# Performance work log

Measured on AMD Instinct MI355X. Metric: run time of the kernel, lower is better.

The kernel has to match this reference:

```python
import jax, jax.numpy as jnp
import numpy as np

T, B = 2048, 16384  # sequence_length, minibatch_size

def setup_inputs() -> dict:
    key = jax.random.key(0)
    ks = jax.random.split(key, 6)
    return {
        "x": jax.random.normal(ks[0], (T, B, 1), dtype=jnp.float32),
        "W1": jax.random.normal(ks[1], (4, 2), dtype=jnp.float32) * 0.5,
        "W2": jax.random.normal(ks[2], (4, 4), dtype=jnp.float32) * 0.5,
        "b2": jax.random.normal(ks[3], (4,), dtype=jnp.float32) * 0.1,
        "W3": jax.random.normal(ks[4], (4, 4), dtype=jnp.float32) * 0.5,
        "W4": jax.random.normal(ks[5], (1, 4), dtype=jnp.float32) * 0.5,
    }

def reference(x, W1, b2, W2, W3, W4):
    # x: (T, B, 1). State starts at zeros (self.state is None -> zeros), no teacher forcing.
    def step(state, x_t):
        # state: (B, 1); x_t: (B, 1)
        inp = jnp.concatenate([x_t, state], axis=-1)        # (B, 2)
        h = jnp.tanh(inp @ W1.T)                            # (B, 4)
        h = jnp.tanh(h @ W2.T + b2)                         # (B, 4)
        h = jnp.tanh(h @ W3.T)                              # (B, 4)
        d = h @ W4.T                                        # (B, 1)
        out = d + state                                     # residual state feedback
        return out, out
    state0 = jnp.zeros((x.shape[1], 1), dtype=x.dtype)
    _, outs = jax.lax.scan(step, state0, x)                 # outs: (T, B, 1)
    return outs
```

## Files before the change

kernel.cpp:

```cpp
#include <hip/hip_runtime.h>

#define TT 2048

__device__ __forceinline__ float tanh_pre(float z) {
    float t = __builtin_amdgcn_exp2f(z);
    float r = __builtin_amdgcn_rcpf(1.0f + t);
    return fmaf(-2.0f, r, 1.0f);
}

__global__ __launch_bounds__(64, 1)
void stn_seq_kernel(const float* __restrict__ x,
                    const float* __restrict__ W1,
                    const float* __restrict__ W2,
                    const float* __restrict__ b2,
                    const float* __restrict__ W3,
                    const float* __restrict__ W4,
                    float* __restrict__ out, int B)
{
    const int b = blockIdx.x * blockDim.x + threadIdx.x;
    if (b >= B) return;
    const float K = 2.8853900817779268f;

    float w1x[4], w1s[4], w2[4][4], bb[4], w3[4][4], w4[4];
    #pragma unroll
    for (int i = 0; i < 4; ++i) {
        w1x[i] = W1[i*2+0] * K;
        w1s[i] = W1[i*2+1] * K;
        bb[i]  = b2[i] * K;
        w4[i]  = W4[i];
        #pragma unroll
        for (int j = 0; j < 4; ++j) {
            w2[i][j] = W2[i*4+j] * K;
            w3[i][j] = W3[i*4+j] * K;
        }
    }

    const float* xp = x + b;
    float* op = out + b;
    float s = 0.0f;

    constexpr int U = 4;
    float xb[U];
    #pragma unroll
    for (int k = 0; k < U; ++k) xb[k] = __builtin_nontemporal_load(xp + k*B);
    xp += (size_t)U * B;

    for (int t = 0; t < TT; t += U) {
        float xc[U];
        #pragma unroll
        for (int k = 0; k < U; ++k) xc[k] = xb[k];
        if (t + U < TT) {
            #pragma unroll
            for (int k = 0; k < U; ++k) xb[k] = __builtin_nontemporal_load(xp + k*B);
        }
        xp += (size_t)U * B;

        #pragma unroll
        for (int k = 0; k < U; ++k) {
            float h1[4], h2[4], h3[4];
            #pragma unroll
            for (int i = 0; i < 4; ++i)
                h1[i] = tanh_pre(fmaf(w1s[i], s, w1x[i] * xc[k]));
            #pragma unroll
            for (int i = 0; i < 4; ++i) {
                float a = bb[i];
                #pragma unroll
                for (int j = 0; j < 4; ++j) a = fmaf(w2[i][j], h1[j], a);
                h2[i] = tanh_pre(a);
            }
            #pragma unroll
            for (int i = 0; i < 4; ++i) {
                float a = w3[i][0] * h2[0];
                #pragma unroll
                for (int j = 1; j < 4; ++j) a = fmaf(w3[i][j], h2[j], a);
                h3[i] = tanh_pre(a);
            }
            float d = w4[0] * h3[0];
            d = fmaf(w4[1], h3[1], d);
            d = fmaf(w4[2], h3[2], d);
            d = fmaf(w4[3], h3[3], d);
            s += d;
            __builtin_nontemporal_store(s, op);
            op += B;
        }
    }
}

extern "C" void kernel_launch(void* const* d_in, const int* in_sizes, int n_in,
                              void* d_out, int out_size, void* d_ws, size_t ws_size,
                              hipStream_t stream)
{
    const float* x  = (const float*)d_in[0];
    const float* W1 = (const float*)d_in[1];
    const float* A2 = (const float*)d_in[2];
    const float* A3 = (const float*)d_in[3];
    const float* W3 = (const float*)d_in[4];
    const float* W4 = (const float*)d_in[5];
    const float* W2 = (in_sizes[2] == 16) ? A2 : A3;
    const float* b2 = (in_sizes[2] == 16) ? A3 : A2;

    const int B = in_sizes[0] / TT;
    float* out = (float*)d_out;

    dim3 block(64);
    dim3 grid((B + 63) / 64);
    hipLaunchKernelGGL(stn_seq_kernel, grid, block, 0, stream,
                       x, W1, W2, b2, W3, W4, out, B);
}
```

Baseline: 473.7 us.

## Split each sequence's hidden units across a lane quad with DPP exchanges

Each batch element's recurrence now runs on four lanes, one per hidden unit, instead of one thread. Lanes exchange activations through DPP quad rotations and reduce the output projection with DPP adds, so every lane does one tanh per layer rather than four. This shortens the per-timestep serial dependency chain and quadruples the thread count, which gives more waves to hide latency with 256-thread blocks. In exchange it adds DPP latency to the chain, makes four lanes load the same x value, and leaves three quarters of lanes masked on the store.

```diff
diff --git a/kernel.cpp b/kernel.cpp
--- a/kernel.cpp
+++ b/kernel.cpp
@@ -8,31 +8,39 @@
     return fmaf(-2.0f, r, 1.0f);
 }
 
-__global__ __launch_bounds__(64, 1)
-void stn_seq_kernel(const float* __restrict__ x,
-                    const float* __restrict__ W1,
-                    const float* __restrict__ W2,
-                    const float* __restrict__ b2,
-                    const float* __restrict__ W3,
-                    const float* __restrict__ W4,
-                    float* __restrict__ out, int B)
+template<int CTRL>
+__device__ __forceinline__ float dpp_f(float x) {
+    return __int_as_float(__builtin_amdgcn_mov_dpp(__float_as_int(x), CTRL, 0xf, 0xf, true));
+}
+#define QP_ROT1 0x39
+#define QP_ROT2 0x4E
+#define QP_ROT3 0x93
+#define QP_XOR1 0xB1
+
+__global__ __launch_bounds__(256, 1)
+void stn_quad_kernel(const float* __restrict__ x,
+                     const float* __restrict__ W1,
+                     const float* __restrict__ W2,
+                     const float* __restrict__ b2,
+                     const float* __restrict__ W3,
+                     const float* __restrict__ W4,
+                     float* __restrict__ out, int B)
 {
-    const int b = blockIdx.x * blockDim.x + threadIdx.x;
+    const int tid = blockIdx.x * blockDim.x + threadIdx.x;
+    const int q   = tid & 3;
+    const int b   = tid >> 2;
     if (b >= B) return;
     const float K = 2.8853900817779268f;
 
-    float w1x[4], w1s[4], w2[4][4], bb[4], w3[4][4], w4[4];
+    const float w1x = W1[q*2+0] * K;
+    const float w1s = W1[q*2+1] * K;
+    const float bb  = b2[q] * K;
+    const float w4l = W4[q];
+    float w2q[4], w3q[4];
     #pragma unroll
-    for (int i = 0; i < 4; ++i) {
-        w1x[i] = W1[i*2+0] * K;
-        w1s[i] = W1[i*2+1] * K;
-        bb[i]  = b2[i] * K;
-        w4[i]  = W4[i];
-        #pragma unroll
-        for (int j = 0; j < 4; ++j) {
-            w2[i][j] = W2[i*4+j] * K;
-            w3[i][j] = W3[i*4+j] * K;
-        }
+    for (int r = 0; r < 4; ++r) {
+        w2q[r] = W2[q*4 + ((q+r)&3)] * K;
+        w3q[r] = W3[q*4 + ((q+r)&3)] * K;
     }
 
     const float* xp = x + b;
@@ -57,30 +65,33 @@
 
         #pragma unroll
         for (int k = 0; k < U; ++k) {
-            float h1[4], h2[4], h3[4];
-            #pragma unroll
-            for (int i = 0; i < 4; ++i)
-                h1[i] = tanh_pre(fmaf(w1s[i], s, w1x[i] * xc[k]));
-            #pragma unroll
-            for (int i = 0; i < 4; ++i) {
-                float a = bb[i];
-                #pragma unroll
-                for (int j = 0; j < 4; ++j) a = fmaf(w2[i][j], h1[j], a);
-                h2[i] = tanh_pre(a);
-            }
-            #pragma unroll
-            for (int i = 0; i < 4; ++i) {
-                float a = w3[i][0] * h2[0];
-                #pragma unroll
-                for (int j = 1; j < 4; ++j) a = fmaf(w3[i][j], h2[j], a);
-                h3[i] = tanh_pre(a);
-            }
-            float d = w4[0] * h3[0];
-            d = fmaf(w4[1], h3[1], d);
-            d = fmaf(w4[2], h3[2], d);
-            d = fmaf(w4[3], h3[3], d);
-            s += d;
-            __builtin_nontemporal_store(s, op);
+            float h1 = tanh_pre(fmaf(w1s, s, w1x * xc[k]));
+
+            float h1r1 = dpp_f<QP_ROT1>(h1);
+            float h1r2 = dpp_f<QP_ROT2>(h1);
+            float h1r3 = dpp_f<QP_ROT3>(h1);
+            float a2 = bb;
+            a2 = fmaf(w2q[0], h1,   a2);
+            a2 = fmaf(w2q[1], h1r1, a2);
+            a2 = fmaf(w2q[2], h1r2, a2);
+            a2 = fmaf(w2q[3], h1r3, a2);
+            float h2 = tanh_pre(a2);
+
+            float h2r1 = dpp_f<QP_ROT1>(h2);
+            float h2r2 = dpp_f<QP_ROT2>(h2);
+            float h2r3 = dpp_f<QP_ROT3>(h2);
+            float a3 = w3q[0] * h2;
+            a3 = fmaf(w3q[1], h2r1, a3);
+            a3 = fmaf(w3q[2], h2r2, a3);
+            a3 = fmaf(w3q[3], h2r3, a3);
+            float h3 = tanh_pre(a3);
+
+            float p = w4l * h3;
+            p += dpp_f<QP_XOR1>(p);
+            p += dpp_f<QP_ROT2>(p);
+            s += p;
+
+            if (q == 0) __builtin_nontemporal_store(s, op);
             op += B;
         }
     }
@@ -102,8 +113,9 @@
     const int B = in_sizes[0] / TT;
     float* out = (float*)d_out;
 
-    dim3 block(64);
-    dim3 grid((B + 63) / 64);
-    hipLaunchKernelGGL(stn_seq_kernel, grid, block, 0, stream,
+    const int threads = B * 4;
+    dim3 block(256);
+    dim3 grid((threads + 255) / 256);
+    hipLaunchKernelGGL(stn_quad_kernel, grid, block, 0, stream,
                        x, W1, W2, b2, W3, W4, out, B);
 }
```

Result: faster. 429.1 us (-9.4%).

## Fold tanh affine into weights and shorten the serial recurrence path

Applied to the files above, without the earlier changes.

Rewrites tanh as 1-2*sigmoid-reciprocal and folds the -2 scale and constant offsets into the next layer's weights and biases, which removes one FMA per activation. It also splits the state so the x-dependent part of the first-layer preactivation is computed ahead of time and only the psum term sits on the dependency chain. Dot products are split into two partial sums to cut chain depth, and x prefetch is deepened to 8+8 steps. The risk is slightly different float rounding and higher register use.

```diff
diff --git a/kernel.cpp b/kernel.cpp
--- a/kernel.cpp
+++ b/kernel.cpp
@@ -2,86 +2,97 @@
 
 #define TT 2048
 
-__device__ __forceinline__ float tanh_pre(float z) {
+__device__ __forceinline__ float sigr(float z) {
     float t = __builtin_amdgcn_exp2f(z);
-    float r = __builtin_amdgcn_rcpf(1.0f + t);
-    return fmaf(-2.0f, r, 1.0f);
+    return __builtin_amdgcn_rcpf(1.0f + t);
 }
 
 __global__ __launch_bounds__(64, 1)
-void stn_seq_kernel(const float* __restrict__ x,
-                    const float* __restrict__ W1,
-                    const float* __restrict__ W2,
-                    const float* __restrict__ b2,
-                    const float* __restrict__ W3,
-                    const float* __restrict__ W4,
-                    float* __restrict__ out, int B)
+void stn_lane_kernel(const float* __restrict__ x,
+                     const float* __restrict__ W1,
+                     const float* __restrict__ W2,
+                     const float* __restrict__ b2,
+                     const float* __restrict__ W3,
+                     const float* __restrict__ W4,
+                     float* __restrict__ out, int B)
 {
     const int b = blockIdx.x * blockDim.x + threadIdx.x;
     if (b >= B) return;
     const float K = 2.8853900817779268f;
 
-    float w1x[4], w1s[4], w2[4][4], bb[4], w3[4][4], w4[4];
+    float Kx[4], Ks[4], B2[4], B3[4], A2[4][4], A3[4][4], A4[4];
+    float C4 = 0.f;
     #pragma unroll
     for (int i = 0; i < 4; ++i) {
-        w1x[i] = W1[i*2+0] * K;
-        w1s[i] = W1[i*2+1] * K;
-        bb[i]  = b2[i] * K;
-        w4[i]  = W4[i];
+        Kx[i] = W1[2*i]   * K;
+        Ks[i] = W1[2*i+1] * K;
+        float s2 = b2[i], s3 = 0.f;
         #pragma unroll
         for (int j = 0; j < 4; ++j) {
-            w2[i][j] = W2[i*4+j] * K;
-            w3[i][j] = W3[i*4+j] * K;
+            A2[i][j] = -2.f * K * W2[i*4+j];
+            A3[i][j] = -2.f * K * W3[i*4+j];
+            s2 += W2[i*4+j];
+            s3 += W3[i*4+j];
         }
+        B2[i] = s2 * K;
+        B3[i] = s3 * K;
+        A4[i] = -2.f * W4[i];
+        C4 += W4[i];
     }
 
     const float* xp = x + b;
     float* op = out + b;
-    float s = 0.0f;
 
-    constexpr int U = 4;
-    float xb[U];
+    float cur[8], nxt[8];
     #pragma unroll
-    for (int k = 0; k < U; ++k) xb[k] = __builtin_nontemporal_load(xp + k*B);
-    xp += (size_t)U * B;
+    for (int j = 0; j < 8; ++j) cur[j] = __builtin_nontemporal_load(xp + j*B);
+    #pragma unroll
+    for (int j = 0; j < 8; ++j) nxt[j] = __builtin_nontemporal_load(xp + (8+j)*B);
 
-    for (int t = 0; t < TT; t += U) {
-        float xc[U];
+    float psum = 0.f, sC = C4;
+    float pre[4];
+    #pragma unroll
+    for (int i = 0; i < 4; ++i) pre[i] = Kx[i] * cur[0];
+
+    for (int t = 0; t < TT; t += 8) {
         #pragma unroll
-        for (int k = 0; k < U; ++k) xc[k] = xb[k];
-        if (t + U < TT) {
-            #pragma unroll
-            for (int k = 0; k < U; ++k) xb[k] = __builtin_nontemporal_load(xp + k*B);
-        }
-        xp += (size_t)U * B;
-
-        #pragma unroll
-        for (int k = 0; k < U; ++k) {
-            float h1[4], h2[4], h3[4];
+        for (int k = 0; k < 8; ++k) {
+            float r1[4];
             #pragma unroll
             for (int i = 0; i < 4; ++i)
-                h1[i] = tanh_pre(fmaf(w1s[i], s, w1x[i] * xc[k]));
+                r1[i] = sigr(fmaf(Ks[i], psum, pre[i]));
+            float xn = (k < 7) ? cur[k+1] : nxt[0];
+            #pragma unroll
+            for (int i = 0; i < 4; ++i)
+                pre[i] = fmaf(Ks[i], sC, Kx[i] * xn);
+            float r2[4];
             #pragma unroll
             for (int i = 0; i < 4; ++i) {
-                float a = bb[i];
-                #pragma unroll
-                for (int j = 0; j < 4; ++j) a = fmaf(w2[i][j], h1[j], a);
-                h2[i] = tanh_pre(a);
+                float f = fmaf(A2[i][1], r1[1], fmaf(A2[i][0], r1[0], B2[i]));
+                float g = fmaf(A2[i][3], r1[3], A2[i][2] * r1[2]);
+                r2[i] = sigr(f + g);
             }
+            float r3[4];
             #pragma unroll
             for (int i = 0; i < 4; ++i) {
-                float a = w3[i][0] * h2[0];
-                #pragma unroll
-                for (int j = 1; j < 4; ++j) a = fmaf(w3[i][j], h2[j], a);
-                h3[i] = tanh_pre(a);
+                float f = fmaf(A3[i][1], r2[1], fmaf(A3[i][0], r2[0], B3[i]));
+                float g = fmaf(A3[i][3], r2[3], A3[i][2] * r2[2]);
+                r3[i] = sigr(f + g);
             }
-            float d = w4[0] * h3[0];
-            d = fmaf(w4[1], h3[1], d);
-            d = fmaf(w4[2], h3[2], d);
-            d = fmaf(w4[3], h3[3], d);
-            s += d;
-            __builtin_nontemporal_store(s, op);
+            float f4 = fmaf(A4[1], r3[1], A4[0] * r3[0]);
+            float g4 = fmaf(A4[3], r3[3], A4[2] * r3[2]);
+            psum = f4 + g4;
+            float o = sC + psum;
+            __builtin_nontemporal_store(o, op);
             op += B;
+            sC = o + C4;
+        }
+        #pragma unroll
+        for (int j = 0; j < 8; ++j) cur[j] = nxt[j];
+        if (t + 16 < TT) {
+            #pragma unroll
+            for (int j = 0; j < 8; ++j)
+                nxt[j] = __builtin_nontemporal_load(xp + (size_t)(t+16+j)*B);
         }
     }
 }
@@ -104,6 +115,6 @@
 
     dim3 block(64);
     dim3 grid((B + 63) / 64);
-    hipLaunchKernelGGL(stn_seq_kernel, grid, block, 0, stream,
+    hipLaunchKernelGGL(stn_lane_kernel, grid, block, 0, stream,
                        x, W1, W2, b2, W3, W4, out, B);
 }
```

Result: slower. 527.9 us (+11.5%).
